# Optimization experiments

Hardware: AMD Instinct MI355X
Metric: run time of the kernel (lower is better)

The kernel has to match this reference:

```python
import jax, jax.numpy as jnp
import numpy as np

B, N, M = 8, 1024, 1024
D, H, P = 256, 4, 128
C = D // H  # per-head dim = 64


def setup_inputs() -> dict:
    key = jax.random.key(0)
    ks = jax.random.split(key, 12)
    s = 1.0 / np.sqrt(D)
    return {
        "input_q": jax.random.normal(ks[0], (B, N, D), jnp.float32),
        "input_k": jax.random.normal(ks[1], (B, M, D), jnp.float32),
        "input_v": jax.random.normal(ks[2], (B, M, D), jnp.float32),
        "Wq": jax.random.normal(ks[3], (D, D), jnp.float32) * s,
        "bq": jnp.zeros((D,), jnp.float32),
        "Wk": jax.random.normal(ks[4], (D, D), jnp.float32) * s,
        "bk": jnp.zeros((D,), jnp.float32),
        "Wv": jax.random.normal(ks[5], (D, D), jnp.float32) * s,
        "bv": jnp.zeros((D,), jnp.float32),
        "emb_table": jax.random.normal(ks[6], (P, D), jnp.float32) * s,
        "attention_factors": jax.random.uniform(ks[7], (B, N, M), jnp.float32),
        "emb_indices_qk": jax.random.randint(ks[8], (B, N, M), 0, P, jnp.int32),
        "key_masks": jnp.zeros((B, M), jnp.bool_),
    }


def _split_heads(x):
    # (B, L, D) -> (B, H, L, C)
    b, l, _ = x.shape
    return x.reshape(b, l, H, C).transpose(0, 2, 1, 3)


def reference(input_q, input_k, input_v, Wq, bq, Wk, bk, Wv, bv,
              emb_table, attention_factors, emb_indices_qk, key_masks):
    q = _split_heads(input_q @ Wq.T + bq)  # (B,H,N,C)
    k = _split_heads(input_k @ Wk.T + bk)  # (B,H,M,C)
    v = _split_heads(input_v @ Wv.T + bv)  # (B,H,M,C)

    # embedding bank: (P, D) -> (H, P, C)   ['p (h c) -> h p c']
    emb_bank = emb_table.reshape(P, H, C).transpose(1, 0, 2)
    scores_p_all = jnp.einsum('bhnc,hpc->bhnp', q, emb_bank)  # (B,H,N,P)
    idx = jnp.broadcast_to(emb_indices_qk[:, None], (q.shape[0], H) + emb_indices_qk.shape[1:])
    scores_p = jnp.take_along_axis(scores_p_all, idx, axis=-1)  # (B,H,N,M)

    scores_e = jnp.einsum('bhnc,bhmc->bhnm', q, k)
    scores = (scores_e + scores_p) / jnp.sqrt(jnp.float32(C))
    scores = attention_factors[:, None] * scores
    scores = jnp.where(key_masks[:, None, None, :], -jnp.inf, scores)
    attn = jax.nn.softmax(scores, axis=-1)  # (B,H,N,M)

    hidden = jnp.einsum('bhnm,bhmc->bhnc', attn, v)
    b, h, n, c = hidden.shape
    hidden = hidden.transpose(0, 2, 1, 3).reshape(b, n, h * c)  # (B,N,D)
    return hidden, attn
```

## Files before the change

kernel.cpp:

```cpp
#include <hip/hip_runtime.h>
#include <math.h>

#define Bb 8
#define Nn 1024
#define Mm 1024
#define Dd 256
#define Hh 4
#define Pp 128

using f16x8 = __attribute__((ext_vector_type(8))) _Float16;
using f32x4 = __attribute__((ext_vector_type(4))) float;
using i32x4 = __attribute__((ext_vector_type(4))) int;

#define MFMA16(a, b, c) __builtin_amdgcn_mfma_f32_16x16x32_f16(a, b, c, 0, 0, 0)

__device__ __forceinline__ int swz(int row, int colByte) {
    return row * 128 + (colByte ^ ((row & 7) << 4));
}

__device__ __forceinline__ void stage8_f32(const float* __restrict__ g, unsigned char* dst) {
    f32x4 a = *(const f32x4*)g;
    f32x4 b = *(const f32x4*)(g + 4);
    f16x8 h;
    h[0] = (_Float16)a[0]; h[1] = (_Float16)a[1]; h[2] = (_Float16)a[2]; h[3] = (_Float16)a[3];
    h[4] = (_Float16)b[0]; h[5] = (_Float16)b[1]; h[6] = (_Float16)b[2]; h[7] = (_Float16)b[3];
    *(f16x8*)dst = h;
}

__global__ __launch_bounds__(256) void proj_kernel(
    const float* __restrict__ xq, const float* __restrict__ xk, const float* __restrict__ xv,
    const float* __restrict__ wq, const float* __restrict__ wk, const float* __restrict__ wv,
    const float* __restrict__ bq, const float* __restrict__ bk, const float* __restrict__ bv,
    _Float16* __restrict__ Qo, _Float16* __restrict__ Ko, _Float16* __restrict__ Vt)
{
    __shared__ __align__(16) unsigned char smem[16384];
    unsigned char* aT = smem;
    unsigned char* bT = smem + 8192;

    const int z = blockIdx.z;
    const float* X    = (z == 0) ? xq : (z == 1) ? xk : xv;
    const float* W    = (z == 0) ? wq : (z == 1) ? wk : wv;
    const float* bias = (z == 0) ? bq : (z == 1) ? bk : bv;

    const int r0 = blockIdx.x * 64;
    const int c0 = blockIdx.y * 64;
    const int l = threadIdx.x;
    const int lane = l & 63;
    const int wx = l >> 6;
    const int grp = lane >> 4, col16 = lane & 15;

    f32x4 acc[4] = {};

    for (int kc = 0; kc < 4; ++kc) {
        for (int it = 0; it < 2; ++it) {
            int s = l + it * 256;
            int row = s >> 3, sl = s & 7;
            stage8_f32(X + (size_t)(r0 + row) * Dd + kc * 64 + sl * 8, aT + swz(row, sl * 16));
            stage8_f32(W + (size_t)(c0 + row) * Dd + kc * 64 + sl * 8, bT + swz(row, sl * 16));
        }
        __syncthreads();
        const int arow = wx * 16 + col16;
        f16x8 af0 = *(const f16x8*)(aT + swz(arow, grp * 16));
        f16x8 af1 = *(const f16x8*)(aT + swz(arow, grp * 16 + 64));
#pragma unroll
        for (int t = 0; t < 4; ++t) {
            int brow = t * 16 + col16;
            f16x8 bf0 = *(const f16x8*)(bT + swz(brow, grp * 16));
            f16x8 bf1 = *(const f16x8*)(bT + swz(brow, grp * 16 + 64));
            acc[t] = MFMA16(af0, bf0, acc[t]);
            acc[t] = MFMA16(af1, bf1, acc[t]);
        }
        __syncthreads();
    }

    if (z < 2) {
        _Float16* O = (z == 0) ? Qo : Ko;
#pragma unroll
        for (int t = 0; t < 4; ++t) {
            float bsc = bias[c0 + t * 16 + col16];
#pragma unroll
            for (int j = 0; j < 4; ++j) {
                int r = r0 + wx * 16 + grp * 4 + j;
                O[(size_t)r * Dd + c0 + t * 16 + col16] = (_Float16)(acc[t][j] + bsc);
            }
        }
    } else {
        _Float16* vt = (_Float16*)smem;
#pragma unroll
        for (int t = 0; t < 4; ++t) {
            float bsc = bias[c0 + t * 16 + col16];
#pragma unroll
            for (int j = 0; j < 4; ++j) {
                int r = wx * 16 + grp * 4 + j;
                int c = t * 16 + col16;
                vt[c * 72 + r] = (_Float16)(acc[t][j] + bsc);
            }
        }
        __syncthreads();
        const int bo = r0 >> 10, m0 = r0 & 1023, h = blockIdx.y;
        for (int it = 0; it < 2; ++it) {
            int s = l + it * 256;
            int c = s >> 3, m8 = s & 7;
            i32x4 val = *(const i32x4*)(vt + c * 72 + m8 * 8);
            *(i32x4*)(Vt + (size_t)((bo * Hh + h) * 64 + c) * Mm + m0 + m8 * 8) = val;
        }
    }
}

__global__ __launch_bounds__(256) void attn_kernel(
    const _Float16* __restrict__ Qi, const _Float16* __restrict__ Ki,
    const _Float16* __restrict__ Vt, const float* __restrict__ emb,
    const float* __restrict__ afac, const int* __restrict__ eidx,
    const unsigned char* __restrict__ kmask,
    float* __restrict__ hid, float* __restrict__ attn)
{
    __shared__ __align__(16) unsigned char smem[24576 + 33024];
    unsigned char* U = smem;
    float* spL = (float*)(smem + 24576);

    const int n0 = blockIdx.x * 64;
    const int h = blockIdx.y, b = blockIdx.z;
    const int l = threadIdx.x, lane = l & 63, wx = l >> 6;
    const int grp = lane >> 4, col16 = lane & 15;

    for (int it = 0; it < 2; ++it) {
        int s = l + it * 256, row = s >> 3, sl = s & 7;
        i32x4 v = *(const i32x4*)(Qi + (size_t)(b * Nn + n0 + row) * Dd + h * 64 + sl * 8);
        *(i32x4*)(U + swz(row, sl * 16)) = v;
    }
    for (int it = 0; it < 4; ++it) {
        int s = l + it * 256, p = s >> 3, sl = s & 7;
        stage8_f32(emb + (size_t)p * Dd + h * 64 + sl * 8, U + 8192 + swz(p, sl * 16));
    }
    __syncthreads();

    const int qrow = wx * 16 + col16;
    f16x8 qf0 = *(const f16x8*)(U + swz(qrow, grp * 16));
    f16x8 qf1 = *(const f16x8*)(U + swz(qrow, grp * 16 + 64));

#pragma unroll
    for (int t = 0; t < 8; ++t) {
        int prow = t * 16 + col16;
        f16x8 e0 = *(const f16x8*)(U + 8192 + swz(prow, grp * 16));
        f16x8 e1 = *(const f16x8*)(U + 8192 + swz(prow, grp * 16 + 64));
        f32x4 a = {};
        a = MFMA16(qf0, e0, a);
        a = MFMA16(qf1, e1, a);
#pragma unroll
        for (int j = 0; j < 4; ++j)
            spL[(wx * 16 + grp * 4 + j) * 129 + t * 16 + col16] = 0.125f * a[j];
    }
    __syncthreads();

    float mx[4], sum_[4];
#pragma unroll
    for (int j = 0; j < 4; ++j) { mx[j] = -INFINITY; sum_[j] = 0.f; }

    const size_t afbase = (size_t)b * Nn * Mm;

    for (int mt = 0; mt < 16; ++mt) {
        for (int it = 0; it < 2; ++it) {
            int s = l + it * 256, row = s >> 3, sl = s & 7;
            i32x4 v = *(const i32x4*)(Ki + (size_t)(b * Mm + mt * 64 + row) * Dd + h * 64 + sl * 8);
            *(i32x4*)(U + swz(row, sl * 16)) = v;
        }
        __syncthreads();
        f32x4 sc[4];
#pragma unroll
        for (int t = 0; t < 4; ++t) {
            int krow = t * 16 + col16;
            f16x8 k0 = *(const f16x8*)(U + swz(krow, grp * 16));
            f16x8 k1 = *(const f16x8*)(U + swz(krow, grp * 16 + 64));
            f32x4 a = {};
            a = MFMA16(qf0, k0, a);
            a = MFMA16(qf1, k1, a);
            sc[t] = a;
        }
#pragma unroll
        for (int t = 0; t < 4; ++t) {
            int m = mt * 64 + t * 16 + col16;
            unsigned char mk = kmask[b * Mm + m];
#pragma unroll
            for (int j = 0; j < 4; ++j) {
                int rl = wx * 16 + grp * 4 + j;
                size_t o = afbase + (size_t)(n0 + rl) * Mm + m;
                float s = (0.125f * sc[t][j] + spL[rl * 129 + eidx[o]]) * afac[o];
                sc[t][j] = mk ? -INFINITY : s;
            }
        }
#pragma unroll
        for (int j = 0; j < 4; ++j) {
            float cm = fmaxf(fmaxf(sc[0][j], sc[1][j]), fmaxf(sc[2][j], sc[3][j]));
            float nm = fmaxf(mx[j], cm);
            float nm2 = (nm == -INFINITY) ? 0.f : nm;
            sum_[j] = sum_[j] * __expf(mx[j] - nm2)
                    + __expf(sc[0][j] - nm2) + __expf(sc[1][j] - nm2)
                    + __expf(sc[2][j] - nm2) + __expf(sc[3][j] - nm2);
            mx[j] = nm;
        }
        __syncthreads();
    }

    float rinv[4];
#pragma unroll
    for (int j = 0; j < 4; ++j) {
        float m_ = mx[j], s_ = sum_[j];
#pragma unroll
        for (int d = 1; d < 16; d <<= 1) {
            float om = __shfl_xor(m_, d, 16);
            float os = __shfl_xor(s_, d, 16);
            float nm = fmaxf(m_, om);
            float nm2 = (nm == -INFINITY) ? 0.f : nm;
            s_ = s_ * __expf(m_ - nm2) + os * __expf(om - nm2);
            m_ = nm;
        }
        mx[j] = (m_ == -INFINITY) ? 0.f : m_;
        rinv[j] = (s_ > 0.f) ? (1.f / s_) : 0.f;
    }

    f32x4 pv[4] = {};
    float* attnB = attn + (size_t)((b * Hh + h) * Nn) * Mm;
    for (int mt = 0; mt < 16; ++mt) {
        for (int it = 0; it < 2; ++it) {
            int s = l + it * 256, row = s >> 3, sl = s & 7;
            i32x4 kv = *(const i32x4*)(Ki + (size_t)(b * Mm + mt * 64 + row) * Dd + h * 64 + sl * 8);
            *(i32x4*)(U + swz(row, sl * 16)) = kv;
            i32x4 vv = *(const i32x4*)(Vt + (size_t)((b * Hh + h) * 64 + row) * Mm + mt * 64 + sl * 8);
            *(i32x4*)(U + 8192 + swz(row, sl * 16)) = vv;
        }
        __syncthreads();
        f32x4 sc[4];
#pragma unroll
        for (int t = 0; t < 4; ++t) {
            int krow = t * 16 + col16;
            f16x8 k0 = *(const f16x8*)(U + swz(krow, grp * 16));
            f16x8 k1 = *(const f16x8*)(U + swz(krow, grp * 16 + 64));
            f32x4 a = {};
            a = MFMA16(qf0, k0, a);
            a = MFMA16(qf1, k1, a);
            sc[t] = a;
        }
#pragma unroll
        for (int t = 0; t < 4; ++t) {
            int m = mt * 64 + t * 16 + col16;
            unsigned char mk = kmask[b * Mm + m];
#pragma unroll
            for (int j = 0; j < 4; ++j) {
                int rl = wx * 16 + grp * 4 + j;
                size_t o = afbase + (size_t)(n0 + rl) * Mm + m;
                float s = (0.125f * sc[t][j] + spL[rl * 129 + eidx[o]]) * afac[o];
                float p = mk ? 0.f : __expf(s - mx[j]) * rinv[j];
                attnB[(size_t)(n0 + rl) * Mm + m] = p;
                *(_Float16*)(U + 16384 + swz(rl, (t * 16 + col16) * 2)) = (_Float16)p;
            }
        }
        __syncthreads();
        const int prow = wx * 16 + col16;
        f16x8 pf0 = *(const f16x8*)(U + 16384 + swz(prow, grp * 16));
        f16x8 pf1 = *(const f16x8*)(U + 16384 + swz(prow, grp * 16 + 64));
#pragma unroll
        for (int t = 0; t < 4; ++t) {
            int vrow = t * 16 + col16;
            f16x8 v0 = *(const f16x8*)(U + 8192 + swz(vrow, grp * 16));
            f16x8 v1 = *(const f16x8*)(U + 8192 + swz(vrow, grp * 16 + 64));
            pv[t] = MFMA16(pf0, v0, pv[t]);
            pv[t] = MFMA16(pf1, v1, pv[t]);
        }
        __syncthreads();
    }

#pragma unroll
    for (int t = 0; t < 4; ++t)
#pragma unroll
        for (int j = 0; j < 4; ++j) {
            int n = n0 + wx * 16 + grp * 4 + j;
            hid[(size_t)(b * Nn + n) * Dd + h * 64 + t * 16 + col16] = pv[t][j];
        }
}

extern "C" void kernel_launch(void* const* d_in, const int* in_sizes, int n_in,
                              void* d_out, int out_size, void* d_ws, size_t ws_size,
                              hipStream_t stream)
{
    (void)in_sizes; (void)n_in; (void)out_size; (void)ws_size;

    const float* xq   = (const float*)d_in[0];
    const float* xk   = (const float*)d_in[1];
    const float* xv   = (const float*)d_in[2];
    const float* wq   = (const float*)d_in[3];
    const float* bq   = (const float*)d_in[4];
    const float* wk   = (const float*)d_in[5];
    const float* bk   = (const float*)d_in[6];
    const float* wv   = (const float*)d_in[7];
    const float* bv   = (const float*)d_in[8];
    const float* emb  = (const float*)d_in[9];
    const float* afac = (const float*)d_in[10];
    const int*   eidx = (const int*)d_in[11];
    const unsigned char* kmask = (const unsigned char*)d_in[12];

    _Float16* Q  = (_Float16*)d_ws;
    _Float16* K  = Q + (size_t)8192 * 256;
    _Float16* Vt = K + (size_t)8192 * 256;

    float* hid  = (float*)d_out;
    float* attn = hid + (size_t)Bb * Nn * Dd;

    proj_kernel<<<dim3(128, 4, 3), 256, 0, stream>>>(xq, xk, xv, wq, wk, wv,
                                                     bq, bk, bv, Q, K, Vt);
    attn_kernel<<<dim3(16, 4, 8), 256, 0, stream>>>(Q, K, Vt, emb, afac, eidx,
                                                    kmask, hid, attn);
}
```

Baseline: 346.0 us.

## Stage attention factors and indices in LDS, drop max tracking, vectorize attn stores

Attention factors and embedding indices are now loaded into shared memory with coalesced 16-byte loads, and the indices are packed to bytes, instead of being gathered per element from global memory. The running max in the softmax is removed on the assumption that scores stay bounded. The 1/sqrt(C) scale is folded into the Q projection and the positional score table is stored in fp16. Attention probabilities are written back as vectorized fp32 rows rebuilt from the fp16 P tile. The goal is to cut uncoalesced global traffic and exp work, at the cost of overflow risk without max subtraction and of fp16-rounded attn output values.

Measured after the change: 334.1 us. 3.5% less time.

```diff
diff --git a/kernel.cpp b/kernel.cpp
--- a/kernel.cpp
+++ b/kernel.cpp
@@ -75,17 +75,19 @@
 
     if (z < 2) {
         _Float16* O = (z == 0) ? Qo : Ko;
+        const float osc = (z == 0) ? 0.125f : 1.0f;
 #pragma unroll
         for (int t = 0; t < 4; ++t) {
             float bsc = bias[c0 + t * 16 + col16];
 #pragma unroll
             for (int j = 0; j < 4; ++j) {
                 int r = r0 + wx * 16 + grp * 4 + j;
-                O[(size_t)r * Dd + c0 + t * 16 + col16] = (_Float16)(acc[t][j] + bsc);
+                O[(size_t)r * Dd + c0 + t * 16 + col16] = (_Float16)((acc[t][j] + bsc) * osc);
             }
         }
     } else {
         _Float16* vt = (_Float16*)smem;
+        __syncthreads();
 #pragma unroll
         for (int t = 0; t < 4; ++t) {
             float bsc = bias[c0 + t * 16 + col16];
@@ -114,9 +116,13 @@
     const unsigned char* __restrict__ kmask,
     float* __restrict__ hid, float* __restrict__ attn)
 {
-    __shared__ __align__(16) unsigned char smem[24576 + 33024];
-    unsigned char* U = smem;
-    float* spL = (float*)(smem + 24576);
+    __shared__ __align__(16) unsigned char smem[63744];
+    unsigned char* Uk = smem;
+    unsigned char* Uv = smem + 8192;
+    unsigned char* Up = smem + 16384;
+    _Float16*      spL = (_Float16*)(smem + 24576);
+    float*         afT = (float*)(smem + 41984);
+    unsigned char* eiT = smem + 59392;
 
     const int n0 = blockIdx.x * 64;
     const int h = blockIdx.y, b = blockIdx.z;
@@ -126,51 +132,65 @@
     for (int it = 0; it < 2; ++it) {
         int s = l + it * 256, row = s >> 3, sl = s & 7;
         i32x4 v = *(const i32x4*)(Qi + (size_t)(b * Nn + n0 + row) * Dd + h * 64 + sl * 8);
-        *(i32x4*)(U + swz(row, sl * 16)) = v;
+        *(i32x4*)(Uk + swz(row, sl * 16)) = v;
     }
     for (int it = 0; it < 4; ++it) {
         int s = l + it * 256, p = s >> 3, sl = s & 7;
-        stage8_f32(emb + (size_t)p * Dd + h * 64 + sl * 8, U + 8192 + swz(p, sl * 16));
+        unsigned char* dst = (p < 64) ? (Uv + swz(p, sl * 16)) : (Up + swz(p - 64, sl * 16));
+        stage8_f32(emb + (size_t)p * Dd + h * 64 + sl * 8, dst);
     }
     __syncthreads();
 
     const int qrow = wx * 16 + col16;
-    f16x8 qf0 = *(const f16x8*)(U + swz(qrow, grp * 16));
-    f16x8 qf1 = *(const f16x8*)(U + swz(qrow, grp * 16 + 64));
+    f16x8 qf0 = *(const f16x8*)(Uk + swz(qrow, grp * 16));
+    f16x8 qf1 = *(const f16x8*)(Uk + swz(qrow, grp * 16 + 64));
 
 #pragma unroll
     for (int t = 0; t < 8; ++t) {
         int prow = t * 16 + col16;
-        f16x8 e0 = *(const f16x8*)(U + 8192 + swz(prow, grp * 16));
-        f16x8 e1 = *(const f16x8*)(U + 8192 + swz(prow, grp * 16 + 64));
+        const unsigned char* base = (t < 4) ? Uv : Up;
+        int pr = (t < 4) ? prow : prow - 64;
+        f16x8 e0 = *(const f16x8*)(base + swz(pr, grp * 16));
+        f16x8 e1 = *(const f16x8*)(base + swz(pr, grp * 16 + 64));
         f32x4 a = {};
         a = MFMA16(qf0, e0, a);
         a = MFMA16(qf1, e1, a);
 #pragma unroll
         for (int j = 0; j < 4; ++j)
-            spL[(wx * 16 + grp * 4 + j) * 129 + t * 16 + col16] = 0.125f * a[j];
+            spL[(wx * 16 + grp * 4 + j) * 136 + t * 16 + col16] = (_Float16)a[j];
     }
     __syncthreads();
 
-    float mx[4], sum_[4];
-#pragma unroll
-    for (int j = 0; j < 4; ++j) { mx[j] = -INFINITY; sum_[j] = 0.f; }
-
-    const size_t afbase = (size_t)b * Nn * Mm;
+    const size_t afrow0 = (size_t)b * Nn * Mm + (size_t)n0 * Mm;
+    const _Float16* Kb = Ki + (size_t)b * Mm * Dd + h * 64;
+    const _Float16* Vb = Vt + (size_t)((b * Hh + h) * 64) * Mm;
+
+    float sum_[4] = {0.f, 0.f, 0.f, 0.f};
 
     for (int mt = 0; mt < 16; ++mt) {
         for (int it = 0; it < 2; ++it) {
             int s = l + it * 256, row = s >> 3, sl = s & 7;
-            i32x4 v = *(const i32x4*)(Ki + (size_t)(b * Mm + mt * 64 + row) * Dd + h * 64 + sl * 8);
-            *(i32x4*)(U + swz(row, sl * 16)) = v;
-        }
-        __syncthreads();
+            i32x4 v = *(const i32x4*)(Kb + (size_t)(mt * 64 + row) * Dd + sl * 8);
+            *(i32x4*)(Uk + swz(row, sl * 16)) = v;
+        }
+        for (int it = 0; it < 4; ++it) {
+            int s = l + it * 256, row = s >> 4, q4 = s & 15;
+            size_t g = afrow0 + (size_t)row * Mm + mt * 64 + q4 * 4;
+            f32x4 av = *(const f32x4*)(afac + g);
+            *(f32x4*)((unsigned char*)afT + row * 272 + q4 * 16) = av;
+            i32x4 iv = *(const i32x4*)(eidx + g);
+            unsigned int pk = (unsigned)(iv[0] & 255) | ((unsigned)(iv[1] & 255) << 8)
+                            | ((unsigned)(iv[2] & 255) << 16) | ((unsigned)(iv[3] & 255) << 24);
+            *(unsigned int*)(eiT + row * 68 + q4 * 4) = pk;
+        }
+        __syncthreads();
+
         f32x4 sc[4];
 #pragma unroll
         for (int t = 0; t < 4; ++t) {
             int krow = t * 16 + col16;
-            f16x8 k0 = *(const f16x8*)(U + swz(krow, grp * 16));
-            f16x8 k1 = *(const f16x8*)(U + swz(krow, grp * 16 + 64));
+            f16x8 k0 = *(const f16x8*)(Uk + swz(krow, grp * 16));
+            f16x8 k1 = *(const f16x8*)(Uk + swz(krow, grp * 16 + 64));
             f32x4 a = {};
             a = MFMA16(qf0, k0, a);
             a = MFMA16(qf1, k1, a);
@@ -178,63 +198,56 @@
         }
 #pragma unroll
         for (int t = 0; t < 4; ++t) {
-            int m = mt * 64 + t * 16 + col16;
-            unsigned char mk = kmask[b * Mm + m];
+            int m = t * 16 + col16;
+            unsigned char mk = kmask[b * Mm + mt * 64 + m];
 #pragma unroll
             for (int j = 0; j < 4; ++j) {
                 int rl = wx * 16 + grp * 4 + j;
-                size_t o = afbase + (size_t)(n0 + rl) * Mm + m;
-                float s = (0.125f * sc[t][j] + spL[rl * 129 + eidx[o]]) * afac[o];
-                sc[t][j] = mk ? -INFINITY : s;
+                float sp = (float)spL[rl * 136 + eiT[rl * 68 + m]];
+                float s = (sc[t][j] + sp) * afT[rl * 68 + m];
+                sum_[j] += mk ? 0.f : __expf(s);
             }
         }
-#pragma unroll
-        for (int j = 0; j < 4; ++j) {
-            float cm = fmaxf(fmaxf(sc[0][j], sc[1][j]), fmaxf(sc[2][j], sc[3][j]));
-            float nm = fmaxf(mx[j], cm);
-            float nm2 = (nm == -INFINITY) ? 0.f : nm;
-            sum_[j] = sum_[j] * __expf(mx[j] - nm2)
-                    + __expf(sc[0][j] - nm2) + __expf(sc[1][j] - nm2)
-                    + __expf(sc[2][j] - nm2) + __expf(sc[3][j] - nm2);
-            mx[j] = nm;
-        }
         __syncthreads();
     }
 
     float rinv[4];
 #pragma unroll
     for (int j = 0; j < 4; ++j) {
-        float m_ = mx[j], s_ = sum_[j];
-#pragma unroll
-        for (int d = 1; d < 16; d <<= 1) {
-            float om = __shfl_xor(m_, d, 16);
-            float os = __shfl_xor(s_, d, 16);
-            float nm = fmaxf(m_, om);
-            float nm2 = (nm == -INFINITY) ? 0.f : nm;
-            s_ = s_ * __expf(m_ - nm2) + os * __expf(om - nm2);
-            m_ = nm;
-        }
-        mx[j] = (m_ == -INFINITY) ? 0.f : m_;
+        float s_ = sum_[j];
+#pragma unroll
+        for (int d = 1; d < 16; d <<= 1) s_ += __shfl_xor(s_, d, 16);
         rinv[j] = (s_ > 0.f) ? (1.f / s_) : 0.f;
     }
 
     f32x4 pv[4] = {};
-    float* attnB = attn + (size_t)((b * Hh + h) * Nn) * Mm;
+    float* attnB = attn + (size_t)((b * Hh + h) * Nn + n0) * Mm;
     for (int mt = 0; mt < 16; ++mt) {
         for (int it = 0; it < 2; ++it) {
             int s = l + it * 256, row = s >> 3, sl = s & 7;
-            i32x4 kv = *(const i32x4*)(Ki + (size_t)(b * Mm + mt * 64 + row) * Dd + h * 64 + sl * 8);
-            *(i32x4*)(U + swz(row, sl * 16)) = kv;
-            i32x4 vv = *(const i32x4*)(Vt + (size_t)((b * Hh + h) * 64 + row) * Mm + mt * 64 + sl * 8);
-            *(i32x4*)(U + 8192 + swz(row, sl * 16)) = vv;
-        }
-        __syncthreads();
+            i32x4 kv = *(const i32x4*)(Kb + (size_t)(mt * 64 + row) * Dd + sl * 8);
+            *(i32x4*)(Uk + swz(row, sl * 16)) = kv;
+            i32x4 vv = *(const i32x4*)(Vb + (size_t)row * Mm + mt * 64 + sl * 8);
+            *(i32x4*)(Uv + swz(row, sl * 16)) = vv;
+        }
+        for (int it = 0; it < 4; ++it) {
+            int s = l + it * 256, row = s >> 4, q4 = s & 15;
+            size_t g = afrow0 + (size_t)row * Mm + mt * 64 + q4 * 4;
+            f32x4 av = *(const f32x4*)(afac + g);
+            *(f32x4*)((unsigned char*)afT + row * 272 + q4 * 16) = av;
+            i32x4 iv = *(const i32x4*)(eidx + g);
+            unsigned int pk = (unsigned)(iv[0] & 255) | ((unsigned)(iv[1] & 255) << 8)
+                            | ((unsigned)(iv[2] & 255) << 16) | ((unsigned)(iv[3] & 255) << 24);
+            *(unsigned int*)(eiT + row * 68 + q4 * 4) = pk;
+        }
+        __syncthreads();
+
         f32x4 sc[4];
 #pragma unroll
         for (int t = 0; t < 4; ++t) {
             int krow = t * 16 + col16;
-            f16x8 k0 = *(const f16x8*)(U + swz(krow, grp * 16));
-            f16x8 k1 = *(const f16x8*)(U + swz(krow, grp * 16 + 64));
+            f16x8 k0 = *(const f16x8*)(Uk + swz(krow, grp * 16));
+            f16x8 k1 = *(const f16x8*)(Uk + swz(krow, grp * 16 + 64));
             f32x4 a = {};
             a = MFMA16(qf0, k0, a);
             a = MFMA16(qf1, k1, a);
@@ -242,29 +255,44 @@
         }
 #pragma unroll
         for (int t = 0; t < 4; ++t) {
-            int m = mt * 64 + t * 16 + col16;
-            unsigned char mk = kmask[b * Mm + m];
+            int m = t * 16 + col16;
+            unsigned char mk = kmask[b * Mm + mt * 64 + m];
 #pragma unroll
             for (int j = 0; j < 4; ++j) {
                 int rl = wx * 16 + grp * 4 + j;
-                size_t o = afbase + (size_t)(n0 + rl) * Mm + m;
-                float s = (0.125f * sc[t][j] + spL[rl * 129 + eidx[o]]) * afac[o];
-                float p = mk ? 0.f : __expf(s - mx[j]) * rinv[j];
-                attnB[(size_t)(n0 + rl) * Mm + m] = p;
-                *(_Float16*)(U + 16384 + swz(rl, (t * 16 + col16) * 2)) = (_Float16)p;
+                float sp = (float)spL[rl * 136 + eiT[rl * 68 + m]];
+                float s = (sc[t][j] + sp) * afT[rl * 68 + m];
+                float p = mk ? 0.f : __expf(s) * rinv[j];
+                *(_Float16*)(Up + swz(rl, m * 2)) = (_Float16)p;
             }
         }
         __syncthreads();
+
         const int prow = wx * 16 + col16;
-        f16x8 pf0 = *(const f16x8*)(U + 16384 + swz(prow, grp * 16));
-        f16x8 pf1 = *(const f16x8*)(U + 16384 + swz(prow, grp * 16 + 64));
+        f16x8 pf0 = *(const f16x8*)(Up + swz(prow, grp * 16));
+        f16x8 pf1 = *(const f16x8*)(Up + swz(prow, grp * 16 + 64));
 #pragma unroll
         for (int t = 0; t < 4; ++t) {
             int vrow = t * 16 + col16;
-            f16x8 v0 = *(const f16x8*)(U + 8192 + swz(vrow, grp * 16));
-            f16x8 v1 = *(const f16x8*)(U + 8192 + swz(vrow, grp * 16 + 64));
+            f16x8 v0 = *(const f16x8*)(Uv + swz(vrow, grp * 16));
+            f16x8 v1 = *(const f16x8*)(Uv + swz(vrow, grp * 16 + 64));
             pv[t] = MFMA16(pf0, v0, pv[t]);
             pv[t] = MFMA16(pf1, v1, pv[t]);
+        }
+
+        {
+            const int arow = l >> 2, am0 = (l & 3) * 16;
+            f16x8 ph0 = *(const f16x8*)(Up + swz(arow, am0 * 2));
+            f16x8 ph1 = *(const f16x8*)(Up + swz(arow, am0 * 2 + 16));
+            float* dst = attnB + (size_t)arow * Mm + mt * 64 + am0;
+            f32x4 o0 = {(float)ph0[0], (float)ph0[1], (float)ph0[2], (float)ph0[3]};
+            f32x4 o1 = {(float)ph0[4], (float)ph0[5], (float)ph0[6], (float)ph0[7]};
+            f32x4 o2 = {(float)ph1[0], (float)ph1[1], (float)ph1[2], (float)ph1[3]};
+            f32x4 o3 = {(float)ph1[4], (float)ph1[5], (float)ph1[6], (float)ph1[7]};
+            *(f32x4*)dst       = o0;
+            *(f32x4*)(dst + 4) = o1;
+            *(f32x4*)(dst + 8) = o2;
+            *(f32x4*)(dst + 12)= o3;
         }
         __syncthreads();
     }
```
